# Optimization experiments

Hardware: AMD Instinct MI355X
Metric: run time of the kernel (lower is better)

Reference implementation:

```python
import jax, jax.numpy as jnp
import numpy as np

EMB_DIM = 2048
N_Q_HEADS = 32
N_KV_HEADS = 8
HEAD_DIM = EMB_DIM // N_Q_HEADS  # 64
N_REP = N_Q_HEADS // N_KV_HEADS  # 4
ROPE_BASE = 10000.0


def setup_inputs() -> dict:
    key = jax.random.key(0)
    ks = jax.random.split(key, 9)
    B, T = 2, 2048
    kv_dim = HEAD_DIM * N_KV_HEADS
    s = 0.02
    return {
        "x":  jax.random.normal(ks[0], (B, T, EMB_DIM), jnp.float32),
        "Wq": jax.random.normal(ks[1], (EMB_DIM, EMB_DIM), jnp.float32) * s,
        "bq": jax.random.normal(ks[2], (EMB_DIM,), jnp.float32) * s,
        "Wk": jax.random.normal(ks[3], (kv_dim, EMB_DIM), jnp.float32) * s,
        "bk": jax.random.normal(ks[4], (kv_dim,), jnp.float32) * s,
        "Wv": jax.random.normal(ks[5], (kv_dim, EMB_DIM), jnp.float32) * s,
        "bv": jax.random.normal(ks[6], (kv_dim,), jnp.float32) * s,
        "Wo": jax.random.normal(ks[7], (EMB_DIM, EMB_DIM), jnp.float32) * s,
        "bo": jax.random.normal(ks[8], (EMB_DIM,), jnp.float32) * s,
    }


def _rope_tables(T, D, dtype):
    inv_freq = 1.0 / (ROPE_BASE ** (jnp.arange(0, D, 2, dtype=jnp.float32) / D))
    t = jnp.arange(T, dtype=jnp.float32)
    freqs = jnp.einsum("i,j->ij", t, inv_freq)          # [T, D/2]
    emb = jnp.concatenate([freqs, freqs], axis=-1)       # [T, D]
    # broadcast over batch and heads: [1, T, 1, D]
    return jnp.cos(emb)[None, :, None, :].astype(dtype), jnp.sin(emb)[None, :, None, :].astype(dtype)


def _rotate_half(x):
    x1, x2 = jnp.split(x, 2, axis=-1)
    return jnp.concatenate([-x2, x1], axis=-1)


def reference(x, Wq, bq, Wk, bk, Wv, bv, Wo, bo):
    B, T, C = x.shape
    q = (x @ Wq.T + bq).reshape(B, T, N_Q_HEADS, HEAD_DIM)
    k = (x @ Wk.T + bk).reshape(B, T, N_KV_HEADS, HEAD_DIM)
    v = (x @ Wv.T + bv).reshape(B, T, N_KV_HEADS, HEAD_DIM)

    cos, sin = _rope_tables(T, HEAD_DIM, x.dtype)
    q = q * cos + _rotate_half(q) * sin
    k = k * cos + _rotate_half(k) * sin

    q = q.transpose(0, 2, 1, 3)                          # [B, Hq, T, D]
    k = k.transpose(0, 2, 1, 3)                          # [B, Hkv, T, D]
    v = v.transpose(0, 2, 1, 3)
    # GQA: repeat_interleave kv heads to match query heads
    k = jnp.repeat(k, N_REP, axis=1)                     # [B, Hq, T, D]
    v = jnp.repeat(v, N_REP, axis=1)

    scale = 1.0 / jnp.sqrt(jnp.asarray(HEAD_DIM, x.dtype))
    att = jnp.einsum("bhqd,bhkd->bhqk", q, k) * scale    # [B, Hq, T, T]
    causal = jnp.tril(jnp.ones((T, T), dtype=bool))
    att = jnp.where(causal[None, None], att, -jnp.inf)
    att = jax.nn.softmax(att, axis=-1)

    y = jnp.einsum("bhqk,bhkd->bhqd", att, v)            # [B, Hq, T, D]
    y = y.transpose(0, 2, 1, 3).reshape(B, T, C)
    return y @ Wo.T + bo
```

## Files before the change

kernel.cpp:

```cpp
#include <hip/hip_runtime.h>
#include <hip/hip_bf16.h>
#include <math.h>


typedef __attribute__((ext_vector_type(8))) short short8;
typedef __attribute__((ext_vector_type(4))) float f32x4;

#define MFMA16(a,b,c) __builtin_amdgcn_mfma_f32_16x16x32_bf16((a),(b),(c),0,0,0)
#define QSCALE 0.18033688011112043f
#define NFREQ  (-13.28771237954945f / 32.0f)

__device__ __forceinline__ ushort f2bf(float f) {
  union { float f; unsigned u; } x; x.f = f;
  unsigned r = x.u + 0x7fffu + ((x.u >> 16) & 1u);
  return (ushort)(r >> 16);
}
__device__ __forceinline__ uint pkbf(float a, float b) {
  union { float f; unsigned u; } x, y; x.f = a; y.f = b;
  return ((x.u + 0x8000u) >> 16) | ((y.u + 0x8000u) & 0xffff0000u);
}

__device__ __forceinline__ void g2l16(const void* g, void* l) {
  __builtin_amdgcn_global_load_lds(
      (__attribute__((address_space(1))) void*)g,
      (__attribute__((address_space(3))) void*)l, 16, 0, 0);
}

__global__ void cvt_all(const float* __restrict__ x,  const float* __restrict__ wq,
                        const float* __restrict__ wk, const float* __restrict__ wv,
                        const float* __restrict__ wo,
                        ushort* __restrict__ x_bf, ushort* __restrict__ wqkv,
                        ushort* __restrict__ wo_bf) {
  int i = blockIdx.x * 256 + threadIdx.x;
  const float4* src; ushort* dst; int off;
  if (i < 2097152)      { src = (const float4*)x;  dst = x_bf;             off = i; }
  else if (i < 3145728) { src = (const float4*)wq; dst = wqkv;             off = i - 2097152; }
  else if (i < 3407872) { src = (const float4*)wk; dst = wqkv + 4194304;   off = i - 3145728; }
  else if (i < 3670016) { src = (const float4*)wv; dst = wqkv + 5242880;   off = i - 3407872; }
  else                  { src = (const float4*)wo; dst = wo_bf;            off = i - 3670016; }
  float4 v = src[off];
  ushort4 o;
  o.x = f2bf(v.x); o.y = f2bf(v.y); o.z = f2bf(v.z); o.w = f2bf(v.w);
  ((ushort4*)dst)[off] = o;
}

__global__ __launch_bounds__(256, 3)
void gemm_qkv(const ushort* __restrict__ A, const ushort* __restrict__ Bw,
              const float* __restrict__ bq, const float* __restrict__ bk,
              const float* __restrict__ bv,
              ushort* __restrict__ qr, ushort* __restrict__ kr,
              ushort* __restrict__ vt) {
  const int K = 2048;
  __shared__ ushort As[2][128*32];
  __shared__ ushort Bs[2][128*32];
  const int tid = threadIdx.x;
  const int wave = tid >> 6, lane = tid & 63;
  const int wm = wave >> 1, wn = wave & 1;
  const int quad = lane >> 4, l16 = lane & 15;
  const int swg = (l16 >> 1) & 3;
  const int m0 = blockIdx.y * 128, n0 = blockIdx.x * 128;

  f32x4 acc[4][4] = {};

  auto stage = [&](int buf, int k0) {
#pragma unroll
    for (int i = 0; i < 2; ++i) {
      int cbase = (i*4 + wave) * 64;
      int p = cbase + lane;
      int row = p >> 2, pcb = p & 3;
      int cl = pcb ^ ((row >> 1) & 3);
      g2l16(A  + (size_t)(m0 + row) * K + k0 + cl * 8, As[buf] + (size_t)cbase * 8);
      g2l16(Bw + (size_t)(n0 + row) * K + k0 + cl * 8, Bs[buf] + (size_t)cbase * 8);
    }
  };

  stage(0, 0);
  for (int k0 = 0; k0 < K; k0 += 32) {
    __syncthreads();
    int cur = (k0 >> 5) & 1;
    if (k0 + 32 < K) stage(cur ^ 1, k0 + 32);

    short8 af[4], bfr[4];
#pragma unroll
    for (int mi = 0; mi < 4; ++mi)
      af[mi] = *(const short8*)(As[cur] + (wm*64 + mi*16 + l16)*32 + ((quad ^ swg) * 8));
#pragma unroll
    for (int ni = 0; ni < 4; ++ni)
      bfr[ni] = *(const short8*)(Bs[cur] + (wn*64 + ni*16 + l16)*32 + ((quad ^ swg) * 8));
#pragma unroll
    for (int mi = 0; mi < 4; ++mi)
#pragma unroll
      for (int ni = 0; ni < 4; ++ni)
        acc[mi][ni] = MFMA16(af[mi], bfr[ni], acc[mi][ni]);
  }

  const int bb = m0 >> 11;
  const int tb = (m0 & 2047) + wm*64;

  if (blockIdx.x < 20) {
    const bool isq = blockIdx.x < 16;
    const float scale = isq ? QSCALE : 1.0f;
#pragma unroll
    for (int ni = 0; ni < 2; ++ni) {
      int n = n0 + wn*64 + ni*16 + l16;
      int d = ni*16 + l16;
      float bias1, bias2;
      ushort* dst;
      if (isq) {
        bias1 = bq[n]; bias2 = bq[n + 32];
        dst = qr + ((size_t)(bb*32 + (n >> 6)) * 2048) * 64 + d;
      } else {
        bias1 = bk[n - 2048]; bias2 = bk[n - 2016];
        dst = kr + ((size_t)(bb*8 + ((n >> 6) - 32)) * 2048) * 64 + d;
      }
      float invf = exp2f((float)d * NFREQ);
#pragma unroll
      for (int mi = 0; mi < 4; ++mi) {
#pragma unroll
        for (int r = 0; r < 4; ++r) {
          int t = tb + mi*16 + quad*4 + r;
          float x1 = acc[mi][ni][r]   + bias1;
          float x2 = acc[mi][ni+2][r] + bias2;
          float f = (float)t * invf;
          float sn = __sinf(f), cs = __cosf(f);
          dst[(size_t)t*64]      = f2bf((x1*cs - x2*sn) * scale);
          dst[(size_t)t*64 + 32] = f2bf((x2*cs + x1*sn) * scale);
        }
      }
    }
  } else {
#pragma unroll
    for (int ni = 0; ni < 4; ++ni) {
      int n = n0 + wn*64 + ni*16 + l16;
      int d = ni*16 + l16;
      float bias = bv[n - 2560];
      ushort* dst = vt + ((size_t)(bb*8 + ((n - 2560) >> 6)) * 64 + d) * 2048;
#pragma unroll
      for (int mi = 0; mi < 4; ++mi) {
        int t = tb + mi*16 + quad*4;
        uint2 pk;
        pk.x = (uint)f2bf(acc[mi][ni][0]+bias) | ((uint)f2bf(acc[mi][ni][1]+bias) << 16);
        pk.y = (uint)f2bf(acc[mi][ni][2]+bias) | ((uint)f2bf(acc[mi][ni][3]+bias) << 16);
        *(uint2*)(dst + t) = pk;
      }
    }
  }
}

__global__ __launch_bounds__(256, 3)
void gemm128(const ushort* __restrict__ A, const ushort* __restrict__ Bw,
             const float* __restrict__ b0,
             float* __restrict__ Cout, int M, int N, int K) {
  __shared__ ushort As[2][128*32];
  __shared__ ushort Bs[2][128*32];
  const int tid = threadIdx.x;
  const int wave = tid >> 6, lane = tid & 63;
  const int wm = wave >> 1, wn = wave & 1;
  const int quad = lane >> 4, l16 = lane & 15;
  const int swg = (l16 >> 1) & 3;
  const int m0 = blockIdx.y * 128, n0 = blockIdx.x * 128;

  f32x4 acc[4][4] = {};

  auto stage = [&](int buf, int k0) {
#pragma unroll
    for (int i = 0; i < 2; ++i) {
      int cbase = (i*4 + wave) * 64;
      int p = cbase + lane;
      int row = p >> 2, pcb = p & 3;
      int cl = pcb ^ ((row >> 1) & 3);
      g2l16(A  + (size_t)(m0 + row) * K + k0 + cl * 8, As[buf] + (size_t)cbase * 8);
      g2l16(Bw + (size_t)(n0 + row) * K + k0 + cl * 8, Bs[buf] + (size_t)cbase * 8);
    }
  };

  stage(0, 0);
  for (int k0 = 0; k0 < K; k0 += 32) {
    __syncthreads();
    int cur = (k0 >> 5) & 1;
    if (k0 + 32 < K) stage(cur ^ 1, k0 + 32);

    short8 af[4], bfr[4];
#pragma unroll
    for (int mi = 0; mi < 4; ++mi)
      af[mi] = *(const short8*)(As[cur] + (wm*64 + mi*16 + l16)*32 + ((quad ^ swg) * 8));
#pragma unroll
    for (int ni = 0; ni < 4; ++ni)
      bfr[ni] = *(const short8*)(Bs[cur] + (wn*64 + ni*16 + l16)*32 + ((quad ^ swg) * 8));
#pragma unroll
    for (int mi = 0; mi < 4; ++mi)
#pragma unroll
      for (int ni = 0; ni < 4; ++ni)
        acc[mi][ni] = MFMA16(af[mi], bfr[ni], acc[mi][ni]);
  }

#pragma unroll
  for (int ni = 0; ni < 4; ++ni) {
    int n = n0 + wn*64 + ni*16 + l16;
    float bias = b0[n];
#pragma unroll
    for (int mi = 0; mi < 4; ++mi) {
#pragma unroll
      for (int r = 0; r < 4; ++r) {
        int m = m0 + wm*64 + mi*16 + quad*4 + r;
        Cout[(size_t)m * N + n] = acc[mi][ni][r] + bias;
      }
    }
  }
}

__global__ __launch_bounds__(256, 4)
void attn(const ushort* __restrict__ Q, const ushort* __restrict__ Kb,
          const ushort* __restrict__ Vt, ushort* __restrict__ Y) {
  __shared__ ushort Ks[2][64*64];
  __shared__ ushort Vs[2][64*64];
  __shared__ ushort Ps[4*16*64];
  const int tid = threadIdx.x, wave = tid >> 6, lane = tid & 63;
  const int quad = lane >> 4, l16 = lane & 15;
  const int h = blockIdx.y, b = blockIdx.z;
  const int hk = h >> 2;
  const ushort* Qb = Q  + ((size_t)(b*32 + h)  * 2048) * 64;
  const ushort* Kg = Kb + ((size_t)(b*8 + hk) * 2048) * 64;
  const ushort* Vg = Vt + ((size_t)(b*8 + hk) * 64) * 2048;
  ushort* Pw = Ps + wave * 1024;
  const int sw = l16 & 7;

  auto stage = [&](int buf, int kt) {
#pragma unroll
    for (int i = 0; i < 2; ++i) {
      int cbase = (i*4 + wave) * 64;
      int p = cbase + lane;
      int row = p >> 3, pcb = p & 7;
      int cl = pcb ^ (row & 7);
      g2l16(Kg + (size_t)(kt*64 + row)*64 + cl*8, Ks[buf] + (size_t)cbase*8);
      g2l16(Vg + (size_t)row*2048 + kt*64 + cl*8, Vs[buf] + (size_t)cbase*8);
    }
  };

  for (int pass = 0; pass < 2; ++pass) {
    const int qt = pass ? (31 - blockIdx.x) : blockIdx.x;
    const int q0 = qt * 64;
    const int qrow = q0 + wave*16 + l16;
    short8 qf0 = *(const short8*)(Qb + (size_t)qrow*64 + quad*8);
    short8 qf1 = *(const short8*)(Qb + (size_t)qrow*64 + 32 + quad*8);

    f32x4 o[4] = {};
    f32x4 l4 = {0.f, 0.f, 0.f, 0.f};

    __syncthreads();
    stage(0, 0);

    for (int kt = 0; kt <= qt; ++kt) {
      __syncthreads();
      int cur = kt & 1;
      if (kt < qt) stage(cur ^ 1, kt + 1);

      f32x4 s[4];
#pragma unroll
      for (int kb = 0; kb < 4; ++kb) {
        const ushort* krow = Ks[cur] + (kb*16 + l16)*64;
        short8 kf0 = *(const short8*)(krow + ((quad       ^ sw) * 8));
        short8 kf1 = *(const short8*)(krow + (((4 + quad) ^ sw) * 8));
        f32x4 z = {0.f, 0.f, 0.f, 0.f};
        z = MFMA16(kf0, qf0, z);
        s[kb] = MFMA16(kf1, qf1, z);
      }

      if (kt == qt) {
        int ql = wave*16 + l16;
#pragma unroll
        for (int kb = 0; kb < 4; ++kb) {
          int keyl = kb*16 + quad*4;
#pragma unroll
          for (int r = 0; r < 4; ++r)
            if (keyl + r > ql) s[kb][r] = -INFINITY;
        }
      }

#pragma unroll
      for (int kb = 0; kb < 4; ++kb)
#pragma unroll
        for (int r = 0; r < 4; ++r)
          s[kb][r] = __builtin_amdgcn_exp2f(s[kb][r]);

      l4 += (s[0] + s[1]) + (s[2] + s[3]);

#pragma unroll
      for (int kb = 0; kb < 4; ++kb) {
        uint2 pk;
        pk.x = pkbf(s[kb][0], s[kb][1]);
        pk.y = pkbf(s[kb][2], s[kb][3]);
        int G = (kb*2 + (quad >> 1)) ^ sw;
        *(uint2*)((char*)Pw + l16*128 + G*16 + (quad & 1)*8) = pk;
      }

#pragma unroll
      for (int kc = 0; kc < 2; ++kc) {
        short8 pf = *(const short8*)((char*)Pw + l16*128 + (((kc*4 + quad) ^ sw) * 16));
#pragma unroll
        for (int db = 0; db < 4; ++db) {
          const ushort* vrow = Vs[cur] + (db*16 + l16)*64;
          short8 vf = *(const short8*)(vrow + (((kc*4 + quad) ^ sw) * 8));
          o[db] = MFMA16(vf, pf, o[db]);
        }
      }
    }

    float l = (l4[0] + l4[1]) + (l4[2] + l4[3]);
    l += __shfl_xor(l, 16);
    l += __shfl_xor(l, 32);
    float inv = 1.0f / l;

    int q = q0 + wave*16 + l16;
#pragma unroll
    for (int db = 0; db < 4; ++db) {
      size_t base = ((size_t)(b*2048 + q)) * 2048 + h*64 + db*16 + quad*4;
      ((uint*)Y)[base >> 1]       = pkbf(o[db][0]*inv, o[db][1]*inv);
      ((uint*)Y)[(base >> 1) + 1] = pkbf(o[db][2]*inv, o[db][3]*inv);
    }
  }
}

extern "C" void kernel_launch(void* const* d_in, const int* in_sizes, int n_in,
                              void* d_out, int out_size, void* d_ws, size_t ws_size,
                              hipStream_t stream) {
  (void)in_sizes; (void)n_in; (void)out_size; (void)ws_size;
  const float* x  = (const float*)d_in[0];
  const float* Wq = (const float*)d_in[1];
  const float* bq = (const float*)d_in[2];
  const float* Wk = (const float*)d_in[3];
  const float* bk = (const float*)d_in[4];
  const float* Wv = (const float*)d_in[5];
  const float* bv = (const float*)d_in[6];
  const float* Wo = (const float*)d_in[7];
  const float* bo = (const float*)d_in[8];
  float* out = (float*)d_out;

  ushort* ws    = (ushort*)d_ws;
  ushort* x_bf  = ws;
  ushort* wqkv  = x_bf + 8388608;
  ushort* wo_bf = wqkv + 6291456;
  ushort* qr    = wo_bf + 4194304;
  ushort* kr    = qr + 8388608;
  ushort* vt    = kr + 2097152;
  ushort* Y     = x_bf;

  cvt_all<<<18432, 256, 0, stream>>>(x, Wq, Wk, Wv, Wo, x_bf, wqkv, wo_bf);
  gemm_qkv<<<dim3(24, 32), 256, 0, stream>>>(x_bf, wqkv, bq, bk, bv, qr, kr, vt);
  attn<<<dim3(16, 32, 2), 256, 0, stream>>>(qr, kr, vt, Y);
  gemm128<<<dim3(16, 32), 256, 0, stream>>>(Y, wo_bf, bo, out, 4096, 2048, 2048);
}
```

Before: 302.3 us.

## Fuse x bf16 conversion into QKV GEMM and process two query tiles per attention block

The separate fp32-to-bf16 conversion of x is removed. The QKV GEMM now loads fp32 x through registers, converts it, and writes it to LDS, overlapped with the MFMA loop. This saves a full write and re-read of the activation. Separately, each attention block now handles a 128-row query tile as two 64-row halves that share every staged K/V tile, which halves K/V LDS traffic per query. In exchange it doubles the register and LDS footprint, lowering occupancy to 2 blocks per CU and halving the number of blocks.

```diff
diff --git a/kernel.cpp b/kernel.cpp
--- a/kernel.cpp
+++ b/kernel.cpp
@@ -26,18 +26,15 @@
       (__attribute__((address_space(3))) void*)l, 16, 0, 0);
 }
 
-__global__ void cvt_all(const float* __restrict__ x,  const float* __restrict__ wq,
-                        const float* __restrict__ wk, const float* __restrict__ wv,
-                        const float* __restrict__ wo,
-                        ushort* __restrict__ x_bf, ushort* __restrict__ wqkv,
-                        ushort* __restrict__ wo_bf) {
+__global__ void cvt_all(const float* __restrict__ wq, const float* __restrict__ wk,
+                        const float* __restrict__ wv, const float* __restrict__ wo,
+                        ushort* __restrict__ wqkv, ushort* __restrict__ wo_bf) {
   int i = blockIdx.x * 256 + threadIdx.x;
   const float4* src; ushort* dst; int off;
-  if (i < 2097152)      { src = (const float4*)x;  dst = x_bf;             off = i; }
-  else if (i < 3145728) { src = (const float4*)wq; dst = wqkv;             off = i - 2097152; }
-  else if (i < 3407872) { src = (const float4*)wk; dst = wqkv + 4194304;   off = i - 3145728; }
-  else if (i < 3670016) { src = (const float4*)wv; dst = wqkv + 5242880;   off = i - 3407872; }
-  else                  { src = (const float4*)wo; dst = wo_bf;            off = i - 3670016; }
+  if (i < 1048576)      { src = (const float4*)wq; dst = wqkv;             off = i; }
+  else if (i < 1310720) { src = (const float4*)wk; dst = wqkv + 4194304;   off = i - 1048576; }
+  else if (i < 1572864) { src = (const float4*)wv; dst = wqkv + 5242880;   off = i - 1310720; }
+  else                  { src = (const float4*)wo; dst = wo_bf;            off = i - 1572864; }
   float4 v = src[off];
   ushort4 o;
   o.x = f2bf(v.x); o.y = f2bf(v.y); o.z = f2bf(v.z); o.w = f2bf(v.w);
@@ -45,7 +42,7 @@
 }
 
 __global__ __launch_bounds__(256, 3)
-void gemm_qkv(const ushort* __restrict__ A, const ushort* __restrict__ Bw,
+void gemm_qkv(const float* __restrict__ X, const ushort* __restrict__ Bw,
               const float* __restrict__ bq, const float* __restrict__ bk,
               const float* __restrict__ bv,
               ushort* __restrict__ qr, ushort* __restrict__ kr,
@@ -60,25 +57,44 @@
   const int swg = (l16 >> 1) & 3;
   const int m0 = blockIdx.y * 128, n0 = blockIdx.x * 128;
 
+  const int arow = tid >> 1, acb = (tid & 1) * 2;
+  const float* aptr = X + (size_t)(m0 + arow) * K + acb * 8;
+  const int acl0 = (acb     ) ^ ((arow >> 1) & 3);
+  const int acl1 = (acb + 1) ^ ((arow >> 1) & 3);
+
   f32x4 acc[4][4] = {};
-
-  auto stage = [&](int buf, int k0) {
+  float4 va0, va1, va2, va3;
+
+  auto loadA = [&](int k0) {
+    const float4* p = (const float4*)(aptr + k0);
+    va0 = p[0]; va1 = p[1]; va2 = p[2]; va3 = p[3];
+  };
+  auto writeA = [&](int buf) {
+    uint4 w0, w1;
+    w0.x = pkbf(va0.x, va0.y); w0.y = pkbf(va0.z, va0.w);
+    w0.z = pkbf(va1.x, va1.y); w0.w = pkbf(va1.z, va1.w);
+    w1.x = pkbf(va2.x, va2.y); w1.y = pkbf(va2.z, va2.w);
+    w1.z = pkbf(va3.x, va3.y); w1.w = pkbf(va3.z, va3.w);
+    *(uint4*)(As[buf] + arow*32 + acl0*8) = w0;
+    *(uint4*)(As[buf] + arow*32 + acl1*8) = w1;
+  };
+  auto stageB = [&](int buf, int k0) {
 #pragma unroll
     for (int i = 0; i < 2; ++i) {
       int cbase = (i*4 + wave) * 64;
       int p = cbase + lane;
       int row = p >> 2, pcb = p & 3;
       int cl = pcb ^ ((row >> 1) & 3);
-      g2l16(A  + (size_t)(m0 + row) * K + k0 + cl * 8, As[buf] + (size_t)cbase * 8);
       g2l16(Bw + (size_t)(n0 + row) * K + k0 + cl * 8, Bs[buf] + (size_t)cbase * 8);
     }
   };
 
-  stage(0, 0);
+  loadA(0); stageB(0, 0); writeA(0);
   for (int k0 = 0; k0 < K; k0 += 32) {
     __syncthreads();
     int cur = (k0 >> 5) & 1;
-    if (k0 + 32 < K) stage(cur ^ 1, k0 + 32);
+    bool more = (k0 + 32) < K;
+    if (more) { loadA(k0 + 32); stageB(cur ^ 1, k0 + 32); }
 
     short8 af[4], bfr[4];
 #pragma unroll
@@ -92,6 +108,8 @@
 #pragma unroll
       for (int ni = 0; ni < 4; ++ni)
         acc[mi][ni] = MFMA16(af[mi], bfr[ni], acc[mi][ni]);
+
+    if (more) writeA(cur ^ 1);
   }
 
   const int bb = m0 >> 11;
@@ -209,20 +227,19 @@
   }
 }
 
-__global__ __launch_bounds__(256, 4)
-void attn(const ushort* __restrict__ Q, const ushort* __restrict__ Kb,
+__global__ __launch_bounds__(256, 2)
+void attn(const ushort* __restrict__ Qm, const ushort* __restrict__ Kb,
           const ushort* __restrict__ Vt, ushort* __restrict__ Y) {
   __shared__ ushort Ks[2][64*64];
   __shared__ ushort Vs[2][64*64];
-  __shared__ ushort Ps[4*16*64];
+  __shared__ ushort Ps[8*16*64];
   const int tid = threadIdx.x, wave = tid >> 6, lane = tid & 63;
   const int quad = lane >> 4, l16 = lane & 15;
   const int h = blockIdx.y, b = blockIdx.z;
   const int hk = h >> 2;
-  const ushort* Qb = Q  + ((size_t)(b*32 + h)  * 2048) * 64;
+  const ushort* Qb = Qm + ((size_t)(b*32 + h)  * 2048) * 64;
   const ushort* Kg = Kb + ((size_t)(b*8 + hk) * 2048) * 64;
   const ushort* Vg = Vt + ((size_t)(b*8 + hk) * 64) * 2048;
-  ushort* Pw = Ps + wave * 1024;
   const int sw = l16 & 7;
 
   auto stage = [&](int buf, int kt) {
@@ -238,85 +255,130 @@
   };
 
   for (int pass = 0; pass < 2; ++pass) {
-    const int qt = pass ? (31 - blockIdx.x) : blockIdx.x;
-    const int q0 = qt * 64;
-    const int qrow = q0 + wave*16 + l16;
-    short8 qf0 = *(const short8*)(Qb + (size_t)qrow*64 + quad*8);
-    short8 qf1 = *(const short8*)(Qb + (size_t)qrow*64 + 32 + quad*8);
-
-    f32x4 o[4] = {};
-    f32x4 l4 = {0.f, 0.f, 0.f, 0.f};
+    const int Q = pass ? (15 - blockIdx.x) : blockIdx.x;
+    const int q0 = Q * 128;
+    const int nkt = 2*Q + 2;
+
+    short8 qf[2][2];
+#pragma unroll
+    for (int qi = 0; qi < 2; ++qi) {
+      int qrow = q0 + qi*64 + wave*16 + l16;
+      qf[qi][0] = *(const short8*)(Qb + (size_t)qrow*64 + quad*8);
+      qf[qi][1] = *(const short8*)(Qb + (size_t)qrow*64 + 32 + quad*8);
+    }
+
+    f32x4 o0[4] = {}, o1[4] = {};
+    f32x4 l40 = {0.f,0.f,0.f,0.f}, l41 = {0.f,0.f,0.f,0.f};
 
     __syncthreads();
     stage(0, 0);
 
-    for (int kt = 0; kt <= qt; ++kt) {
+    for (int kt = 0; kt < nkt; ++kt) {
       __syncthreads();
       int cur = kt & 1;
-      if (kt < qt) stage(cur ^ 1, kt + 1);
-
-      f32x4 s[4];
+      bool f0 = kt <= 2*Q;
+      if (kt + 1 < nkt) stage(cur ^ 1, kt + 1);
+
+      f32x4 s0[4], s1[4];
 #pragma unroll
       for (int kb = 0; kb < 4; ++kb) {
         const ushort* krow = Ks[cur] + (kb*16 + l16)*64;
         short8 kf0 = *(const short8*)(krow + ((quad       ^ sw) * 8));
         short8 kf1 = *(const short8*)(krow + (((4 + quad) ^ sw) * 8));
-        f32x4 z = {0.f, 0.f, 0.f, 0.f};
-        z = MFMA16(kf0, qf0, z);
-        s[kb] = MFMA16(kf1, qf1, z);
-      }
-
-      if (kt == qt) {
-        int ql = wave*16 + l16;
+        if (f0) {
+          f32x4 z = {0.f,0.f,0.f,0.f};
+          z = MFMA16(kf0, qf[0][0], z);
+          s0[kb] = MFMA16(kf1, qf[0][1], z);
+        }
+        f32x4 z1 = {0.f,0.f,0.f,0.f};
+        z1 = MFMA16(kf0, qf[1][0], z1);
+        s1[kb] = MFMA16(kf1, qf[1][1], z1);
+      }
+
+      int ql = wave*16 + l16;
+      if (kt == 2*Q) {
 #pragma unroll
         for (int kb = 0; kb < 4; ++kb) {
           int keyl = kb*16 + quad*4;
 #pragma unroll
           for (int r = 0; r < 4; ++r)
-            if (keyl + r > ql) s[kb][r] = -INFINITY;
-        }
-      }
-
+            if (keyl + r > ql) s0[kb][r] = -INFINITY;
+        }
+      }
+      if (kt == 2*Q + 1) {
+#pragma unroll
+        for (int kb = 0; kb < 4; ++kb) {
+          int keyl = kb*16 + quad*4;
+#pragma unroll
+          for (int r = 0; r < 4; ++r)
+            if (keyl + r > ql) s1[kb][r] = -INFINITY;
+        }
+      }
+
+      ushort* Pw0 = Ps + (wave*2 + 0) * 1024;
+      ushort* Pw1 = Ps + (wave*2 + 1) * 1024;
+
+      if (f0) {
+#pragma unroll
+        for (int kb = 0; kb < 4; ++kb)
+#pragma unroll
+          for (int r = 0; r < 4; ++r)
+            s0[kb][r] = __builtin_amdgcn_exp2f(s0[kb][r]);
+        l40 += (s0[0] + s0[1]) + (s0[2] + s0[3]);
+#pragma unroll
+        for (int kb = 0; kb < 4; ++kb) {
+          uint2 pk;
+          pk.x = pkbf(s0[kb][0], s0[kb][1]);
+          pk.y = pkbf(s0[kb][2], s0[kb][3]);
+          int G = (kb*2 + (quad >> 1)) ^ sw;
+          *(uint2*)((char*)Pw0 + l16*128 + G*16 + (quad & 1)*8) = pk;
+        }
+      }
 #pragma unroll
       for (int kb = 0; kb < 4; ++kb)
 #pragma unroll
         for (int r = 0; r < 4; ++r)
-          s[kb][r] = __builtin_amdgcn_exp2f(s[kb][r]);
-
-      l4 += (s[0] + s[1]) + (s[2] + s[3]);
-
+          s1[kb][r] = __builtin_amdgcn_exp2f(s1[kb][r]);
+      l41 += (s1[0] + s1[1]) + (s1[2] + s1[3]);
 #pragma unroll
       for (int kb = 0; kb < 4; ++kb) {
         uint2 pk;
-        pk.x = pkbf(s[kb][0], s[kb][1]);
-        pk.y = pkbf(s[kb][2], s[kb][3]);
+        pk.x = pkbf(s1[kb][0], s1[kb][1]);
+        pk.y = pkbf(s1[kb][2], s1[kb][3]);
         int G = (kb*2 + (quad >> 1)) ^ sw;
-        *(uint2*)((char*)Pw + l16*128 + G*16 + (quad & 1)*8) = pk;
+        *(uint2*)((char*)Pw1 + l16*128 + G*16 + (quad & 1)*8) = pk;
       }
 
 #pragma unroll
       for (int kc = 0; kc < 2; ++kc) {
-        short8 pf = *(const short8*)((char*)Pw + l16*128 + (((kc*4 + quad) ^ sw) * 16));
+        short8 pf0;
+        if (f0) pf0 = *(const short8*)((char*)Pw0 + l16*128 + (((kc*4 + quad) ^ sw) * 16));
+        short8 pf1 = *(const short8*)((char*)Pw1 + l16*128 + (((kc*4 + quad) ^ sw) * 16));
 #pragma unroll
         for (int db = 0; db < 4; ++db) {
           const ushort* vrow = Vs[cur] + (db*16 + l16)*64;
           short8 vf = *(const short8*)(vrow + (((kc*4 + quad) ^ sw) * 8));
-          o[db] = MFMA16(vf, pf, o[db]);
-        }
-      }
-    }
-
-    float l = (l4[0] + l4[1]) + (l4[2] + l4[3]);
-    l += __shfl_xor(l, 16);
-    l += __shfl_xor(l, 32);
-    float inv = 1.0f / l;
-
-    int q = q0 + wave*16 + l16;
-#pragma unroll
-    for (int db = 0; db < 4; ++db) {
-      size_t base = ((size_t)(b*2048 + q)) * 2048 + h*64 + db*16 + quad*4;
-      ((uint*)Y)[base >> 1]       = pkbf(o[db][0]*inv, o[db][1]*inv);
-      ((uint*)Y)[(base >> 1) + 1] = pkbf(o[db][2]*inv, o[db][3]*inv);
+          if (f0) o0[db] = MFMA16(vf, pf0, o0[db]);
+          o1[db] = MFMA16(vf, pf1, o1[db]);
+        }
+      }
+    }
+
+#pragma unroll
+    for (int qi = 0; qi < 2; ++qi) {
+      f32x4 l4 = qi ? l41 : l40;
+      f32x4* o = qi ? o1 : o0;
+      float l = (l4[0] + l4[1]) + (l4[2] + l4[3]);
+      l += __shfl_xor(l, 16);
+      l += __shfl_xor(l, 32);
+      float inv = 1.0f / l;
+      int q = q0 + qi*64 + wave*16 + l16;
+#pragma unroll
+      for (int db = 0; db < 4; ++db) {
+        size_t base = ((size_t)(b*2048 + q)) * 2048 + h*64 + db*16 + quad*4;
+        ((uint*)Y)[base >> 1]       = pkbf(o[db][0]*inv, o[db][1]*inv);
+        ((uint*)Y)[(base >> 1) + 1] = pkbf(o[db][2]*inv, o[db][3]*inv);
+      }
     }
   }
 }
@@ -337,16 +399,15 @@
   float* out = (float*)d_out;
 
   ushort* ws    = (ushort*)d_ws;
-  ushort* x_bf  = ws;
-  ushort* wqkv  = x_bf + 8388608;
+  ushort* wqkv  = ws;
   ushort* wo_bf = wqkv + 6291456;
   ushort* qr    = wo_bf + 4194304;
   ushort* kr    = qr + 8388608;
   ushort* vt    = kr + 2097152;
-  ushort* Y     = x_bf;
-
-  cvt_all<<<18432, 256, 0, stream>>>(x, Wq, Wk, Wv, Wo, x_bf, wqkv, wo_bf);
-  gemm_qkv<<<dim3(24, 32), 256, 0, stream>>>(x_bf, wqkv, bq, bk, bv, qr, kr, vt);
-  attn<<<dim3(16, 32, 2), 256, 0, stream>>>(qr, kr, vt, Y);
+  ushort* Y     = vt + 2097152;
+
+  cvt_all<<<10240, 256, 0, stream>>>(Wq, Wk, Wv, Wo, wqkv, wo_bf);
+  gemm_qkv<<<dim3(24, 32), 256, 0, stream>>>(x, wqkv, bq, bk, bv, qr, kr, vt);
+  attn<<<dim3(8, 32, 2), 256, 0, stream>>>(qr, kr, vt, Y);
   gemm128<<<dim3(16, 32), 256, 0, stream>>>(Y, wo_bf, bo, out, 4096, 2048, 2048);
 }
```

Result: slower. 346.1 us (+14.5%).
